# Optimization experiments

Measured on AMD Instinct MI355X. Metric: run time of the kernel, lower is better.

Reference implementation:

```python
import jax, jax.numpy as jnp
import numpy as np

B, H, W = 32, 64, 64
C1, C2, K = 32, 64, 5
FC1 = 512
FLAT = C2 * H * W  # 262144


def setup_inputs() -> dict:
    key = jax.random.key(0)
    ks = jax.random.split(key, 9)
    return {
        "x": jax.random.normal(ks[0], (B, 1, H, W), dtype=jnp.float32),
        "w1r": jax.random.normal(ks[1], (C1, 1, K, K), dtype=jnp.float32),
        "w1i": jax.random.normal(ks[2], (C1, 1, K, K), dtype=jnp.float32),
        "w2r": jax.random.normal(ks[3], (C2, C1, K, K), dtype=jnp.float32),
        "w2i": jax.random.normal(ks[4], (C2, C1, K, K), dtype=jnp.float32),
        "fc1_w": jax.random.normal(ks[5], (FC1, FLAT), dtype=jnp.float32) * 0.01,
        "fc1_b": jax.random.normal(ks[6], (FC1,), dtype=jnp.float32),
        "fc2_w": jax.random.normal(ks[7], (10, FC1), dtype=jnp.float32) * 0.05,
        "fc2_b": jax.random.normal(ks[8], (10,), dtype=jnp.float32),
    }


def freq_conv(x, wr, wi):
    # kernel: (out, in, K, K) complex, zero-padded to (out, in, H, W), FFT2'd once
    # (the torch code redundantly tiles this per batch; math is identical)
    kern = wr + 1j * wi  # complex64
    h, w = x.shape[-2], x.shape[-1]
    kern_pad = jnp.pad(kern, ((0, 0), (0, 0), (0, h - K), (0, w - K)))
    kf = jnp.fft.fft2(kern_pad)  # (out, in, H, W) complex64
    # fused multiply + sum over in_channels: (B,in,H,W) x (out,in,H,W) -> (B,out,H,W)
    return jnp.einsum("bihw,oihw->bohw", x.astype(jnp.complex64), kf)


def reference(x, w1r, w1i, w2r, w2i, fc1_w, fc1_b, fc2_w, fc2_b):
    h1 = jnp.abs(freq_conv(x, w1r, w1i))          # (B, C1, H, W) float32
    h2 = jnp.abs(freq_conv(h1, w2r, w2i))         # (B, C2, H, W) float32
    flat = h2.reshape(h2.shape[0], -1)            # (B, FLAT)
    y = flat @ fc1_w.T + fc1_b                    # (B, FC1)
    return y @ fc2_w.T + fc2_b                    # (B, 10)
```

## Files before the change

kernel.cpp:

```cpp
#include <hip/hip_runtime.h>
#include <math.h>

#define PI2 6.283185307179586f


__global__ void k1_a1(const float* __restrict__ w1r, const float* __restrict__ w1i,
                      float* __restrict__ a1) {
    int idx = blockIdx.x * 256 + threadIdx.x;
    int i  = idx >> 12;
    int hw = idx & 4095;
    int u = hw >> 6, v = hw & 63;
    const float* wr = w1r + i * 25;
    const float* wi = w1i + i * 25;
    float re = 0.f, im = 0.f;
    #pragma unroll
    for (int p = 0; p < 5; ++p) {
        #pragma unroll
        for (int q = 0; q < 5; ++q) {
            float s, c;
            sincosf(-(PI2 / 64.f) * (float)((u * p + v * q) & 63), &s, &c);
            float ar = wr[p * 5 + q], ai = wi[p * 5 + q];
            re += ar * c - ai * s;
            im += ar * s + ai * c;
        }
    }
    a1[idx] = sqrtf(re * re + im * im);
}

__global__ void k2a_G(const float* __restrict__ w2r, const float* __restrict__ w2i,
                      float* __restrict__ G) {
    int idx = blockIdx.x * 256 + threadIdx.x;
    int v  = idx & 63;
    int p  = (idx >> 6) % 5;
    int oi = idx / 320;
    const float* wr = w2r + oi * 25 + p * 5;
    const float* wi = w2i + oi * 25 + p * 5;
    float re = 0.f, im = 0.f;
    #pragma unroll
    for (int q = 0; q < 5; ++q) {
        float s, c;
        sincosf(-(PI2 / 64.f) * (float)((v * q) & 63), &s, &c);
        re += wr[q] * c - wi[q] * s;
        im += wr[q] * s + wi[q] * c;
    }
    G[2 * idx]     = re;
    G[2 * idx + 1] = im;
}

__global__ void k2b_t(const float* __restrict__ G, const float* __restrict__ a1,
                      float* __restrict__ t) {
    __shared__ float Gs[10240];
    int o  = blockIdx.x >> 2;
    int ug = blockIdx.x & 3;
    const float* Go = G + o * 20480;
    float re[4] = {0.f, 0.f, 0.f, 0.f};
    float im[4] = {0.f, 0.f, 0.f, 0.f};
    for (int half = 0; half < 2; ++half) {
        __syncthreads();
        for (int jj = threadIdx.x; jj < 10240; jj += 256)
            Gs[jj] = Go[half * 10240 + jj];
        __syncthreads();
        #pragma unroll
        for (int jt = 0; jt < 4; ++jt) {
            int j = jt * 256 + threadIdx.x;
            int u = ug * 16 + (j >> 6);
            int v = j & 63;
            float cu[5], su[5];
            #pragma unroll
            for (int p = 0; p < 5; ++p)
                sincosf(-(PI2 / 64.f) * (float)((u * p) & 63), &su[p], &cu[p]);
            #pragma unroll 4
            for (int i = 0; i < 16; ++i) {
                float a = a1[(half * 16 + i) * 4096 + u * 64 + v];
                float sr = 0.f, si = 0.f;
                #pragma unroll
                for (int p = 0; p < 5; ++p) {
                    float gr = Gs[2 * ((i * 5 + p) * 64 + v)];
                    float gi = Gs[2 * ((i * 5 + p) * 64 + v) + 1];
                    sr += gr * cu[p] - gi * su[p];
                    si += gr * su[p] + gi * cu[p];
                }
                re[jt] += a * sr;
                im[jt] += a * si;
            }
        }
    }
    #pragma unroll
    for (int jt = 0; jt < 4; ++jt) {
        int j = jt * 256 + threadIdx.x;
        int u = ug * 16 + (j >> 6);
        int v = j & 63;
        t[o * 4096 + u * 64 + v] = sqrtf(re[jt] * re[jt] + im[jt] * im[jt]);
    }
}

__global__ __launch_bounds__(256) void k3_y1(
        const float* __restrict__ fc1_w, const float* __restrict__ t,
        const float* __restrict__ x, float* __restrict__ y1) {
    int f  = blockIdx.x >> 2;
    int hb = blockIdx.x & 3;
    int hw = hb * 1024 + threadIdx.x * 4;
    const float4* wrow = (const float4*)(fc1_w + (size_t)f * 262144);
    float4 acc = make_float4(0.f, 0.f, 0.f, 0.f);
    #pragma unroll 4
    for (int o = 0; o < 64; ++o) {
        float4 wv = wrow[(o * 4096 + hw) >> 2];
        float4 tv = *(const float4*)(t + o * 4096 + hw);
        acc.x += tv.x * wv.x;
        acc.y += tv.y * wv.y;
        acc.z += tv.z * wv.z;
        acc.w += tv.w * wv.w;
    }
    float part[32];
    #pragma unroll
    for (int b = 0; b < 32; ++b) {
        float4 xv = *(const float4*)(x + b * 4096 + hw);
        part[b] = acc.x * fabsf(xv.x) + acc.y * fabsf(xv.y)
                + acc.z * fabsf(xv.z) + acc.w * fabsf(xv.w);
    }
    #pragma unroll
    for (int b = 0; b < 32; ++b) {
        #pragma unroll
        for (int m = 32; m >= 1; m >>= 1)
            part[b] += __shfl_xor(part[b], m, 64);
    }
    __shared__ float red[4][32];
    int wave = threadIdx.x >> 6;
    int lane = threadIdx.x & 63;
    if (lane == 0) {
        #pragma unroll
        for (int b = 0; b < 32; ++b) red[wave][b] = part[b];
    }
    __syncthreads();
    if (threadIdx.x < 32) {
        float s = red[0][threadIdx.x] + red[1][threadIdx.x]
                + red[2][threadIdx.x] + red[3][threadIdx.x];
        atomicAdd(&y1[threadIdx.x * 512 + f], s);
    }
}

__global__ void k4_out(const float* __restrict__ y1, const float* __restrict__ fc1_b,
                       const float* __restrict__ fc2_w, const float* __restrict__ fc2_b,
                       float* __restrict__ out) {
    int tid = threadIdx.x;
    if (tid >= 320) return;
    int b = tid / 10, c = tid % 10;
    float acc = fc2_b[c];
    for (int f = 0; f < 512; ++f)
        acc += fc2_w[c * 512 + f] * (y1[b * 512 + f] + fc1_b[f]);
    out[b * 10 + c] = acc;
}

extern "C" void kernel_launch(void* const* d_in, const int* in_sizes, int n_in,
                              void* d_out, int out_size, void* d_ws, size_t ws_size,
                              hipStream_t stream) {
    const float* x    = (const float*)d_in[0];
    const float* w1r  = (const float*)d_in[1];
    const float* w1i  = (const float*)d_in[2];
    const float* w2r  = (const float*)d_in[3];
    const float* w2i  = (const float*)d_in[4];
    const float* fc1w = (const float*)d_in[5];
    const float* fc1b = (const float*)d_in[6];
    const float* fc2w = (const float*)d_in[7];
    const float* fc2b = (const float*)d_in[8];
    float* out = (float*)d_out;

    float* a1 = (float*)d_ws;
    float* G  = a1 + 131072;
    float* t  = G + 1310720;
    float* y1 = t + 262144;

    hipMemsetAsync(y1, 0, 16384 * sizeof(float), stream);
    k1_a1<<<512, 256, 0, stream>>>(w1r, w1i, a1);
    k2a_G<<<2560, 256, 0, stream>>>(w2r, w2i, G);
    k2b_t<<<256, 256, 0, stream>>>(G, a1, t);
    k3_y1<<<2048, 256, 0, stream>>>(fc1w, t, x, y1);
    k4_out<<<1, 320, 0, stream>>>(y1, fc1b, fc2w, fc2b, out);
}
```

Baseline: 797.2 us.

## Merge weight-FFT kernels, split G planes, process two fc1 rows per block

Merges the two small weight-transform kernels into one launch and stores G as separate real and imaginary planes, so shared-memory reads in k2b_t become stride-1. The fc1 kernel now handles two output features per block using nontemporal loads of the 1 GB weight matrix. It also reduces each batch's partial sum inside the loop instead of holding 32 partials in registers, which lowers register pressure. The fc1 weight stream dominates, so most of the expected effect comes from the streaming pattern and from reusing each t load for two rows.

```diff
diff --git a/kernel.cpp b/kernel.cpp
--- a/kernel.cpp
+++ b/kernel.cpp
@@ -3,62 +3,67 @@
 
 #define PI2 6.283185307179586f
 
+typedef float floatx4 __attribute__((ext_vector_type(4)));
 
-__global__ void k1_a1(const float* __restrict__ w1r, const float* __restrict__ w1i,
-                      float* __restrict__ a1) {
-    int idx = blockIdx.x * 256 + threadIdx.x;
-    int i  = idx >> 12;
-    int hw = idx & 4095;
-    int u = hw >> 6, v = hw & 63;
-    const float* wr = w1r + i * 25;
-    const float* wi = w1i + i * 25;
-    float re = 0.f, im = 0.f;
-    #pragma unroll
-    for (int p = 0; p < 5; ++p) {
+
+__global__ void kA_small(const float* __restrict__ w1r, const float* __restrict__ w1i,
+                         const float* __restrict__ w2r, const float* __restrict__ w2i,
+                         float* __restrict__ a1, float* __restrict__ G_re,
+                         float* __restrict__ G_im) {
+    if (blockIdx.x < 512) {
+        int idx = blockIdx.x * 256 + threadIdx.x;
+        int i  = idx >> 12;
+        int hw = idx & 4095;
+        int u = hw >> 6, v = hw & 63;
+        const float* wr = w1r + i * 25;
+        const float* wi = w1i + i * 25;
+        float re = 0.f, im = 0.f;
+        #pragma unroll
+        for (int p = 0; p < 5; ++p) {
+            #pragma unroll
+            for (int q = 0; q < 5; ++q) {
+                float s, c;
+                sincosf(-(PI2 / 64.f) * (float)((u * p + v * q) & 63), &s, &c);
+                float ar = wr[p * 5 + q], ai = wi[p * 5 + q];
+                re += ar * c - ai * s;
+                im += ar * s + ai * c;
+            }
+        }
+        a1[idx] = sqrtf(re * re + im * im);
+    } else {
+        int idx = (blockIdx.x - 512) * 256 + threadIdx.x;
+        int v  = idx & 63;
+        int p  = (idx >> 6) % 5;
+        int oi = idx / 320;
+        const float* wr = w2r + oi * 25 + p * 5;
+        const float* wi = w2i + oi * 25 + p * 5;
+        float re = 0.f, im = 0.f;
         #pragma unroll
         for (int q = 0; q < 5; ++q) {
             float s, c;
-            sincosf(-(PI2 / 64.f) * (float)((u * p + v * q) & 63), &s, &c);
-            float ar = wr[p * 5 + q], ai = wi[p * 5 + q];
-            re += ar * c - ai * s;
-            im += ar * s + ai * c;
+            sincosf(-(PI2 / 64.f) * (float)((v * q) & 63), &s, &c);
+            re += wr[q] * c - wi[q] * s;
+            im += wr[q] * s + wi[q] * c;
         }
+        G_re[idx] = re;
+        G_im[idx] = im;
     }
-    a1[idx] = sqrtf(re * re + im * im);
 }
 
-__global__ void k2a_G(const float* __restrict__ w2r, const float* __restrict__ w2i,
-                      float* __restrict__ G) {
-    int idx = blockIdx.x * 256 + threadIdx.x;
-    int v  = idx & 63;
-    int p  = (idx >> 6) % 5;
-    int oi = idx / 320;
-    const float* wr = w2r + oi * 25 + p * 5;
-    const float* wi = w2i + oi * 25 + p * 5;
-    float re = 0.f, im = 0.f;
-    #pragma unroll
-    for (int q = 0; q < 5; ++q) {
-        float s, c;
-        sincosf(-(PI2 / 64.f) * (float)((v * q) & 63), &s, &c);
-        re += wr[q] * c - wi[q] * s;
-        im += wr[q] * s + wi[q] * c;
-    }
-    G[2 * idx]     = re;
-    G[2 * idx + 1] = im;
-}
-
-__global__ void k2b_t(const float* __restrict__ G, const float* __restrict__ a1,
-                      float* __restrict__ t) {
-    __shared__ float Gs[10240];
+__global__ void k2b_t(const float* __restrict__ G_re, const float* __restrict__ G_im,
+                      const float* __restrict__ a1, float* __restrict__ t) {
+    __shared__ float Gsr[5120];
+    __shared__ float Gsi[5120];
     int o  = blockIdx.x >> 2;
     int ug = blockIdx.x & 3;
-    const float* Go = G + o * 20480;
     float re[4] = {0.f, 0.f, 0.f, 0.f};
     float im[4] = {0.f, 0.f, 0.f, 0.f};
     for (int half = 0; half < 2; ++half) {
         __syncthreads();
-        for (int jj = threadIdx.x; jj < 10240; jj += 256)
-            Gs[jj] = Go[half * 10240 + jj];
+        for (int jj = threadIdx.x; jj < 5120; jj += 256) {
+            Gsr[jj] = G_re[o * 10240 + half * 5120 + jj];
+            Gsi[jj] = G_im[o * 10240 + half * 5120 + jj];
+        }
         __syncthreads();
         #pragma unroll
         for (int jt = 0; jt < 4; ++jt) {
@@ -75,8 +80,8 @@
                 float sr = 0.f, si = 0.f;
                 #pragma unroll
                 for (int p = 0; p < 5; ++p) {
-                    float gr = Gs[2 * ((i * 5 + p) * 64 + v)];
-                    float gi = Gs[2 * ((i * 5 + p) * 64 + v) + 1];
+                    float gr = Gsr[(i * 5 + p) * 64 + v];
+                    float gi = Gsi[(i * 5 + p) * 64 + v];
                     sr += gr * cu[p] - gi * su[p];
                     si += gr * su[p] + gi * cu[p];
                 }
@@ -97,45 +102,42 @@
 __global__ __launch_bounds__(256) void k3_y1(
         const float* __restrict__ fc1_w, const float* __restrict__ t,
         const float* __restrict__ x, float* __restrict__ y1) {
-    int f  = blockIdx.x >> 2;
+    int f0 = (blockIdx.x >> 2) * 2;
     int hb = blockIdx.x & 3;
     int hw = hb * 1024 + threadIdx.x * 4;
-    const float4* wrow = (const float4*)(fc1_w + (size_t)f * 262144);
-    float4 acc = make_float4(0.f, 0.f, 0.f, 0.f);
-    #pragma unroll 4
+    const floatx4* w0 = (const floatx4*)(fc1_w + (size_t)f0 * 262144);
+    const floatx4* w1 = (const floatx4*)(fc1_w + (size_t)(f0 + 1) * 262144);
+    floatx4 acc0 = (floatx4)(0.f);
+    floatx4 acc1 = (floatx4)(0.f);
+    #pragma unroll 8
     for (int o = 0; o < 64; ++o) {
-        float4 wv = wrow[(o * 4096 + hw) >> 2];
-        float4 tv = *(const float4*)(t + o * 4096 + hw);
-        acc.x += tv.x * wv.x;
-        acc.y += tv.y * wv.y;
-        acc.z += tv.z * wv.z;
-        acc.w += tv.w * wv.w;
+        int e = (o * 4096 + hw) >> 2;
+        floatx4 tv = *(const floatx4*)(t + o * 4096 + hw);
+        floatx4 wa = __builtin_nontemporal_load(w0 + e);
+        floatx4 wb = __builtin_nontemporal_load(w1 + e);
+        acc0 += tv * wa;
+        acc1 += tv * wb;
     }
-    float part[32];
-    #pragma unroll
-    for (int b = 0; b < 32; ++b) {
-        float4 xv = *(const float4*)(x + b * 4096 + hw);
-        part[b] = acc.x * fabsf(xv.x) + acc.y * fabsf(xv.y)
-                + acc.z * fabsf(xv.z) + acc.w * fabsf(xv.w);
-    }
-    #pragma unroll
-    for (int b = 0; b < 32; ++b) {
-        #pragma unroll
-        for (int m = 32; m >= 1; m >>= 1)
-            part[b] += __shfl_xor(part[b], m, 64);
-    }
-    __shared__ float red[4][32];
+    __shared__ float red[4][32][2];
     int wave = threadIdx.x >> 6;
     int lane = threadIdx.x & 63;
-    if (lane == 0) {
+    for (int b = 0; b < 32; ++b) {
+        floatx4 xv = *(const floatx4*)(x + b * 4096 + hw);
+        float ax = fabsf(xv.x), ay = fabsf(xv.y), az = fabsf(xv.z), aw = fabsf(xv.w);
+        float p0 = acc0.x * ax + acc0.y * ay + acc0.z * az + acc0.w * aw;
+        float p1 = acc1.x * ax + acc1.y * ay + acc1.z * az + acc1.w * aw;
         #pragma unroll
-        for (int b = 0; b < 32; ++b) red[wave][b] = part[b];
+        for (int m = 32; m >= 1; m >>= 1) {
+            p0 += __shfl_xor(p0, m, 64);
+            p1 += __shfl_xor(p1, m, 64);
+        }
+        if (lane == 0) { red[wave][b][0] = p0; red[wave][b][1] = p1; }
     }
     __syncthreads();
-    if (threadIdx.x < 32) {
-        float s = red[0][threadIdx.x] + red[1][threadIdx.x]
-                + red[2][threadIdx.x] + red[3][threadIdx.x];
-        atomicAdd(&y1[threadIdx.x * 512 + f], s);
+    if (threadIdx.x < 64) {
+        int b = threadIdx.x >> 1, ff = threadIdx.x & 1;
+        float s = red[0][b][ff] + red[1][b][ff] + red[2][b][ff] + red[3][b][ff];
+        atomicAdd(&y1[b * 512 + f0 + ff], s);
     }
 }
 
@@ -165,15 +167,15 @@
     const float* fc2b = (const float*)d_in[8];
     float* out = (float*)d_out;
 
-    float* a1 = (float*)d_ws;
-    float* G  = a1 + 131072;
-    float* t  = G + 1310720;
-    float* y1 = t + 262144;
+    float* a1   = (float*)d_ws;
+    float* G_re = a1 + 131072;
+    float* G_im = G_re + 655360;
+    float* t    = G_im + 655360;
+    float* y1   = t + 262144;
 
-    hipMemsetAsync(y1, 0, 16384 * sizeof(float), stream);
-    k1_a1<<<512, 256, 0, stream>>>(w1r, w1i, a1);
-    k2a_G<<<2560, 256, 0, stream>>>(w2r, w2i, G);
-    k2b_t<<<256, 256, 0, stream>>>(G, a1, t);
-    k3_y1<<<2048, 256, 0, stream>>>(fc1w, t, x, y1);
+    (void)hipMemsetAsync(y1, 0, 16384 * sizeof(float), stream);
+    kA_small<<<3072, 256, 0, stream>>>(w1r, w1i, w2r, w2i, a1, G_re, G_im);
+    k2b_t<<<256, 256, 0, stream>>>(G_re, G_im, a1, t);
+    k3_y1<<<1024, 256, 0, stream>>>(fc1w, t, x, y1);
     k4_out<<<1, 320, 0, stream>>>(y1, fc1b, fc2w, fc2b, out);
 }
```

Measured after the change: 768.0 us. -3.7%, faster.
